# Optimization experiments

Hardware: AMD Instinct MI355X
Metric: run time of the kernel (lower is better)

Reference implementation:

```python
import jax, jax.numpy as jnp
import numpy as np


def _sin_rpe(Lq, d_model, dtype):
    # sinusoidal relative-position embeddings for positions -(Lq-1)..(Lq-1)
    inv_freq = 1.0 / (10000.0 ** (jnp.arange(0, d_model, 2, dtype=jnp.float32) / d_model))
    pos = jnp.arange(-(Lq - 1), Lq, dtype=jnp.float32)  # [2Lq-1]
    ang = pos[:, None] * inv_freq[None, :]               # [2Lq-1, d_model/2]
    emb = jnp.zeros((2 * Lq - 1, d_model), dtype=jnp.float32)
    emb = emb.at[:, 0::2].set(jnp.sin(ang)).at[:, 1::2].set(jnp.cos(ang))
    return emb.astype(dtype)


def _rel_shift(x):
    # Transformer-XL relative shift. x: [B,H,Lq,Lr] with Lr = 2Lq-1
    B, H, Lq, Lr = x.shape
    xp = jnp.concatenate([jnp.zeros((B, H, Lq, 1), x.dtype), x], axis=-1)
    xp = xp.reshape(B, H, Lr + 1, Lq)
    return xp[:, :, 1:].reshape(B, H, Lq, Lr)[..., Lr - Lq:]


def setup_inputs() -> dict:
    key = jax.random.key(0)
    ks = jax.random.split(key, 7)
    B, Lq, D, H = 1, 2048, 1024, 16
    d_head = D // H
    s = 0.02
    return {
        "w": jax.random.normal(ks[0], (B, Lq, D), jnp.float32),
        "Wq": jax.random.normal(ks[1], (D, D), jnp.float32) * s,
        "Wk": jax.random.normal(ks[2], (D, D), jnp.float32) * s,
        "Wv": jax.random.normal(ks[3], (D, D), jnp.float32) * s,
        "Wr": jax.random.normal(ks[4], (D, D), jnp.float32) * s,
        "u_bias": jax.random.normal(ks[5], (H, d_head), jnp.float32) * 0.02,
        "v_bias": jax.random.normal(ks[6], (H, d_head), jnp.float32) * 0.02,
    }


def reference(w, Wq, Wk, Wv, Wr, u_bias, v_bias):
    B, Lq, D = w.shape
    H, d_head = u_bias.shape
    scale = 1.0 / np.sqrt(d_head).astype(np.float32)
    r = _sin_rpe(Lq, D, w.dtype)                          # [2Lq-1, D]
    # torch Linear: y = x @ W.T
    q = (w @ Wq.T).reshape(B, Lq, H, d_head).transpose(0, 2, 1, 3)  # [B,H,Lq,d]
    k = (w @ Wk.T).reshape(B, Lq, H, d_head).transpose(0, 2, 1, 3)
    v = (w @ Wv.T).reshape(B, Lq, H, d_head).transpose(0, 2, 1, 3)
    rp = (r @ Wr.T).reshape(2 * Lq - 1, H, d_head).transpose(1, 0, 2)  # [H,2Lq-1,d]
    AC = jnp.einsum('bhid,bhjd->bhij', q + u_bias[None, :, None, :], k)   # [B,H,Lq,Lq]
    BD = jnp.einsum('bhid,hjd->bhij', q + v_bias[None, :, None, :], rp)   # [B,H,Lq,2Lq-1]
    BD = _rel_shift(BD)                                                   # [B,H,Lq,Lq]
    attn = jax.nn.softmax((AC + BD) * scale, axis=-1)
    out = jnp.einsum('bhij,bhjd->bhid', attn, v)          # [B,H,Lq,d]
    return out.transpose(0, 2, 1, 3).reshape(B, Lq, D)
```

## Files before the change

### kernel.cpp

```cpp
#include <hip/hip_runtime.h>
#include <math.h>
#include <stddef.h>

#define LQ 2048
#define DM 1024
#define NH 16
#define DH 64
#define LR 4095

typedef __attribute__((ext_vector_type(4))) float f4v;
typedef __attribute__((ext_vector_type(8))) short s8v;
typedef __attribute__((ext_vector_type(2))) unsigned short us2;
typedef __attribute__((ext_vector_type(8))) unsigned short us8;
typedef __attribute__((ext_vector_type(2))) unsigned int u32x2;
typedef __attribute__((ext_vector_type(4))) unsigned int u32x4;

__device__ __forceinline__ unsigned short f2bf(float x) {
    unsigned int u = __float_as_uint(x);
    return (unsigned short)((u + 0x7FFFu + ((u >> 16) & 1u)) >> 16);
}
__device__ __forceinline__ float bf2f(unsigned short s) {
    return __uint_as_float(((unsigned int)s) << 16);
}
__device__ __forceinline__ unsigned cvtpk(float lo, float hi) {
    unsigned r;
    asm("v_cvt_pk_bf16_f32 %0, %1, %2" : "=v"(r) : "v"(lo), "v"(hi));
    return r;
}
template<int CTRL>
__device__ __forceinline__ float rot16(float x) {
    return __uint_as_float((unsigned)__builtin_amdgcn_update_dpp(
        0, (int)__float_as_uint(x), CTRL, 0xF, 0xF, false));
}
#define GLOAD16(g, l) __builtin_amdgcn_global_load_lds((g), (l), 16, 0, 0)
#define WAVE_LDS_FENCE() do { \
    asm volatile("s_waitcnt lgkmcnt(0)" ::: "memory"); \
    __builtin_amdgcn_sched_barrier(0); } while (0)

#define MFMA16(a, b, c) __builtin_amdgcn_mfma_f32_16x16x32_bf16((a), (b), (c), 0, 0, 0)

__device__ __forceinline__ s8v sw_read8(const unsigned short* base, int row, int colshort) {
    int byte = (row * 128 + colshort * 2) ^ ((row & 7) << 4);
    return *(const s8v*)((const char*)base + byte);
}

__global__ __launch_bounds__(256)
void prep(const float* __restrict__ w, const float* __restrict__ Wq,
          const float* __restrict__ Wk, const float* __restrict__ Wv,
          const float* __restrict__ Wr, unsigned short* __restrict__ dst,
          unsigned short* __restrict__ r, unsigned short* __restrict__ rpg) {
    int b = blockIdx.x;
    if (b < 3072) {
        size_t e0 = ((size_t)b * 256 + threadIdx.x) * 8;
        const float* src;
        if (e0 < (size_t)LQ * DM) src = w + e0;
        else {
            size_t ro = e0 - (size_t)LQ * DM;
            int wi = (int)(ro >> 20);
            size_t off = ro & 1048575;
            src = (wi == 0 ? Wq : wi == 1 ? Wk : wi == 2 ? Wv : Wr) + off;
        }
        f4v a = *(const f4v*)src;
        f4v c = *(const f4v*)(src + 4);
        us8 o;
        o[0]=f2bf(a[0]); o[1]=f2bf(a[1]); o[2]=f2bf(a[2]); o[3]=f2bf(a[3]);
        o[4]=f2bf(c[0]); o[5]=f2bf(c[1]); o[6]=f2bf(c[2]); o[7]=f2bf(c[3]);
        *(us8*)(dst + e0) = o;
    } else if (b < 11262) {
        int tg = (b - 3072) * 256 + threadIdx.x;
        int gm = tg >> 9, c2 = tg & 511;
        float invf = expf(-(float)c2 * (9.210340371976184f / 512.0f));
        float ang = (float)(gm - (LQ - 1)) * invf;
        us2 o; o[0] = f2bf(sinf(ang)); o[1] = f2bf(cosf(ang));
        *(us2*)&r[(size_t)gm * DM + c2 * 2] = o;
    } else {
        int idx = (b - 11262) * 2048 + threadIdx.x * 8;
        unsigned short* p = (idx < 131072)
            ? (rpg - 131072 + idx)
            : (rpg + (size_t)LR * DM + (idx - 131072));
        *(us8*)p = (us8){0,0,0,0,0,0,0,0};
    }
}

__global__ __launch_bounds__(256)
void proj_all(const unsigned short* __restrict__ wbf, const unsigned short* __restrict__ rr,
              const unsigned short* __restrict__ Wqb, const unsigned short* __restrict__ Wkb,
              const unsigned short* __restrict__ Wvb, const unsigned short* __restrict__ Wrb,
              unsigned short* __restrict__ qb, unsigned short* __restrict__ kkb,
              unsigned short* __restrict__ vtg, unsigned short* __restrict__ rpg) {
    __shared__ unsigned short ldsbuf[2 * 128 * 64];
    unsigned short* As = ldsbuf;
    unsigned short* Bs = ldsbuf + 128 * 64;
    int bid = blockIdx.x;
    int mat, mblk, nblk;
    if (bid < 384) { mat = bid >> 7; int rm = bid & 127; mblk = rm >> 3; nblk = rm & 7; }
    else           { mat = 3; int rm = bid - 384; mblk = rm >> 3; nblk = rm & 7; }
    const int M = (mat < 3) ? LQ : LR;
    const unsigned short* A = (mat < 3) ? wbf : rr;
    const unsigned short* B = mat == 0 ? Wqb : mat == 1 ? Wkb : mat == 2 ? Wvb : Wrb;
    unsigned short* C = mat == 0 ? qb : mat == 1 ? kkb : mat == 2 ? vtg : rpg;
    const int m0 = mblk * 128, n0 = nblk * 128;
    const int t = threadIdx.x;
    const int w = t >> 6, lan16 = t & 15, lgrp = (t & 63) >> 4;
    const int wm = (w >> 1) * 64, wn = (w & 1) * 64;
    f4v acc[4][4] = {};

    for (int k0 = 0; k0 < DM; k0 += 64) {
        #pragma unroll
        for (int it = 0; it < 4; ++it) {
            int slot = it * 256 + t;
            int row = slot >> 3, c8 = slot & 7;
            int gm = m0 + row; if (gm > M - 1) gm = M - 1;
            GLOAD16(A + (size_t)gm * DM + k0 + c8 * 8,
                    (char*)As + (size_t)(it * 256 + (t & ~63)) * 16);
            GLOAD16(B + (size_t)(n0 + row) * DM + k0 + c8 * 8,
                    (char*)Bs + (size_t)(it * 256 + (t & ~63)) * 16);
        }
        __syncthreads();
        #pragma unroll
        for (int kk = 0; kk < 2; ++kk) {
            s8v aF[4], bF[4];
            #pragma unroll
            for (int i = 0; i < 4; ++i) {
                aF[i] = *(const s8v*)&As[(wm + i * 16 + lan16) * 64 + kk * 32 + lgrp * 8];
                bF[i] = *(const s8v*)&Bs[(wn + i * 16 + lan16) * 64 + kk * 32 + lgrp * 8];
            }
            #pragma unroll
            for (int i = 0; i < 4; ++i)
                #pragma unroll
                for (int j = 0; j < 4; ++j)
                    acc[i][j] = MFMA16(aF[i], bF[j], acc[i][j]);
        }
        __syncthreads();
    }
    if (mat != 2) {
        #pragma unroll
        for (int i = 0; i < 4; ++i)
            #pragma unroll
            for (int j = 0; j < 4; ++j)
                #pragma unroll
                for (int rg = 0; rg < 4; ++rg) {
                    int row = m0 + wm + i * 16 + lgrp * 4 + rg;
                    if (row < M)
                        C[(size_t)row * DM + n0 + wn + j * 16 + lan16] = f2bf(acc[i][j][rg]);
                }
    } else {
        unsigned short* Ct = ldsbuf;
        #pragma unroll
        for (int i = 0; i < 4; ++i)
            #pragma unroll
            for (int j = 0; j < 4; ++j) {
                int n = wn + j * 16 + lan16;
                int mb = wm + i * 16 + lgrp * 4;
                int byte = (n * 256 + mb * 2) ^ ((n & 7) << 4);
                u32x2 pp;
                pp[0] = cvtpk(acc[i][j][0], acc[i][j][1]);
                pp[1] = cvtpk(acc[i][j][2], acc[i][j][3]);
                *(u32x2*)((char*)Ct + byte) = pp;
            }
        __syncthreads();
        #pragma unroll
        for (int it = 0; it < 8; ++it) {
            int slot = it * 256 + t;
            int n = slot >> 4, c8 = slot & 15;
            int byte = (n * 256 + c8 * 16) ^ ((n & 7) << 4);
            us8 v = *(const us8*)((const char*)Ct + byte);
            *(us8*)&C[(size_t)(n0 + n) * LQ + m0 + c8 * 8] = v;
        }
    }
}

__global__ __launch_bounds__(256, 2)
void attn_mfma(const unsigned short* __restrict__ q, const unsigned short* __restrict__ kkg,
               const unsigned short* __restrict__ vtg, const unsigned short* __restrict__ rpg,
               const float* __restrict__ ub, const float* __restrict__ vb,
               float* __restrict__ out) {
    __shared__ unsigned short Kb[2][64 * 64];
    __shared__ unsigned short Bb[2][128 * 64];
    __shared__ unsigned short Vb[64 * 64];
    __shared__ unsigned short Gtw[4][80 * 20];
    __shared__ unsigned short Pt[4][64 * 18];

    const int dd = blockIdx.x;
    const int f = (dd & 7) * 64 + (dd >> 3);
    const int h = f >> 5;
    const int i0 = (f & 31) * 64;
    const int col0 = h * DH;

    const int t = threadIdx.x;
    const int w = t >> 6, lan16 = t & 15, lgrp = (t & 63) >> 4;
    const int W = w * 16;
    const int cbase = 48 - W;
    const float C1 = 0.125f * 1.4426950408889634f;
    const float C0 = -4.0f * 1.4426950408889634f;

    unsigned short* gw = Gtw[w];
    unsigned short* pw = Pt[w];

    union uv { u32x4 u; s8v s; };
    auto mkfrag = [&](int gi, const float* bias, s8v* dstf) {
        #pragma unroll
        for (int kk = 0; kk < 2; ++kk) {
            int cb = kk * 32 + lgrp * 8;
            us8 qv = (us8){0,0,0,0,0,0,0,0};
            if (gi < LQ) qv = *(const us8*)(q + (size_t)gi * DM + col0 + cb);
            f4v b0 = *(const f4v*)(bias + col0 + cb);
            f4v b1 = *(const f4v*)(bias + col0 + cb + 4);
            uv o;
            o.u[0] = cvtpk(bf2f(qv[0]) + b0[0], bf2f(qv[1]) + b0[1]);
            o.u[1] = cvtpk(bf2f(qv[2]) + b0[2], bf2f(qv[3]) + b0[3]);
            o.u[2] = cvtpk(bf2f(qv[4]) + b1[0], bf2f(qv[5]) + b1[1]);
            o.u[3] = cvtpk(bf2f(qv[6]) + b1[2], bf2f(qv[7]) + b1[3]);
            dstf[kk] = o.s;
        }
    };
    s8v quF[2], qvlF[2], qvsF[2];
    mkfrag(i0 + W + lan16, ub, quF);
    mkfrag(i0 + W + lan16, vb, qvlF);
    mkfrag(i0 + W + 1 + lan16, vb, qvsF);

    auto stageK = [&](int j0, int buf) {
        #pragma unroll
        for (int it = 0; it < 2; ++it) {
            int slot = it * 256 + t;
            int row = slot >> 3, c8 = (t & 7) ^ (row & 7);
            GLOAD16(kkg + (size_t)(j0 + row) * DM + col0 + c8 * 8,
                    (char*)&Kb[buf][0] + (size_t)(it * 256 + (t & ~63)) * 16);
        }
    };
    auto stageB = [&](int rel, int buf) {
        int base = (rel <= 0) ? rel + 4031 : rel - 65;
        #pragma unroll
        for (int it = 0; it < 4; ++it) {
            int slot = it * 256 + t;
            int row = slot >> 3, c8 = (t & 7) ^ (row & 7);
            GLOAD16(rpg + (ptrdiff_t)(base + row) * DM + col0 + c8 * 8,
                    (char*)&Bb[buf][0] + (size_t)(it * 256 + (t & ~63)) * 16);
        }
    };
    auto stageV = [&](int j0) {
        #pragma unroll
        for (int it = 0; it < 2; ++it) {
            int slot = it * 256 + t;
            int row = slot >> 3, c8 = (t & 7) ^ (row & 7);
            GLOAD16(vtg + (size_t)(col0 + row) * LQ + j0 + c8 * 8,
                    (char*)&Vb[0] + (size_t)(it * 256 + (t & ~63)) * 16);
        }
    };

    f4v accO[4] = {};
    float lsum[4] = {0.f, 0.f, 0.f, 0.f};

    stageK(0, 0);
    stageB(0 - i0, 0);

    auto tile_body = [&](int tt, int cur) {
        const int j0 = tt * 64;
        const int rel = j0 - i0;
        stageV(j0);
        const int tn = (tt < 31) ? tt + 1 : 31;
        stageK(tn * 64, cur ^ 1);
        stageB(tn * 64 - i0, cur ^ 1);
        __builtin_amdgcn_sched_barrier(0);
        asm volatile("s_waitcnt vmcnt(8)" ::: "memory");
        __builtin_amdgcn_s_barrier();
        __builtin_amdgcn_sched_barrier(0);

        __builtin_amdgcn_s_setprio(1);
        f4v acF[4] = {};
        #pragma unroll
        for (int nf = 0; nf < 4; ++nf)
            #pragma unroll
            for (int kk = 0; kk < 2; ++kk) {
                s8v bF = sw_read8(&Kb[cur][0], nf * 16 + lan16, kk * 32 + lgrp * 8);
                acF[nf] = MFMA16(quF[kk], bF, acF[nf]);
            }
        f4v g[5] = {};
        {
            const s8v* qf = (rel <= 0) ? qvlF : qvsF;
            #pragma unroll
            for (int c = 0; c < 5; ++c)
                #pragma unroll
                for (int kk = 0; kk < 2; ++kk) {
                    s8v bF = sw_read8(&Bb[cur][0], cbase + c * 16 + lan16, kk * 32 + lgrp * 8);
                    g[c] = MFMA16(qf[kk], bF, g[c]);
                }
        }
        __builtin_amdgcn_s_setprio(0);
        if (rel == 0) {
            #pragma unroll
            for (int c = 0; c < 5; ++c) {
                int trow = -65 + cbase + c * 16 + lan16;
                const unsigned short* bp = rpg + (ptrdiff_t)trow * DM + col0;
                #pragma unroll
                for (int kk = 0; kk < 2; ++kk) {
                    us8 bv = *(const us8*)(bp + kk * 32 + lgrp * 8);
                    g[c] = MFMA16(qvsF[kk], (s8v)bv, g[c]);
                }
            }
        }
        #pragma unroll
        for (int c = 0; c < 5; ++c) {
            int cl = c * 16 + lan16;
            u32x2 pp;
            pp[0] = cvtpk(g[c][0], g[c][1]);
            pp[1] = cvtpk(g[c][2], g[c][3]);
            *(u32x2*)&gw[cl * 20 + lgrp * 4] = pp;
        }
        WAVE_LDS_FENCE();

        #pragma unroll
        for (int nf = 0; nf < 4; ++nf) {
            int jl = nf * 16 + lan16;
            float pp[4];
            #pragma unroll
            for (int rg = 0; rg < 4; ++rg) {
                const int rhat = lgrp * 4 + rg;
                float bd = bf2f(gw[(jl - rhat + 15) * 20 + rhat]);
                pp[rg] = exp2f(fmaf(acF[nf][rg] + bd, C1, C0));
                lsum[rg] += pp[rg];
            }
            *(unsigned*)&pw[jl * 18 + lgrp * 4]     = cvtpk(pp[0], pp[1]);
            *(unsigned*)&pw[jl * 18 + lgrp * 4 + 2] = cvtpk(pp[2], pp[3]);
        }
        WAVE_LDS_FENCE();

        s8v pF[2];
        #pragma unroll
        for (int kk = 0; kk < 2; ++kk) {
            us8 tmp;
            #pragma unroll
            for (int e = 0; e < 8; ++e)
                tmp[e] = pw[(kk * 32 + lgrp * 8 + e) * 18 + lan16];
            pF[kk] = (s8v)tmp;
        }
        __builtin_amdgcn_sched_barrier(0);
        asm volatile("s_waitcnt vmcnt(6)" ::: "memory");
        __builtin_amdgcn_s_barrier();
        __builtin_amdgcn_sched_barrier(0);

        __builtin_amdgcn_s_setprio(1);
        #pragma unroll
        for (int nf = 0; nf < 4; ++nf)
            #pragma unroll
            for (int kk = 0; kk < 2; ++kk) {
                s8v vF = sw_read8(&Vb[0], nf * 16 + lan16, kk * 32 + lgrp * 8);
                accO[nf] = MFMA16(pF[kk], vF, accO[nf]);
            }
        __builtin_amdgcn_s_setprio(0);
        __builtin_amdgcn_sched_barrier(0);
        __builtin_amdgcn_s_barrier();
        __builtin_amdgcn_sched_barrier(0);
    };

    #pragma unroll 1
    for (int tp = 0; tp < 16; ++tp) {
        tile_body(tp * 2, 0);
        tile_body(tp * 2 + 1, 1);
    }

    #pragma unroll
    for (int rg = 0; rg < 4; ++rg) {
        float s = lsum[rg];
        s += rot16<0x121>(s);
        s += rot16<0x122>(s);
        s += rot16<0x124>(s);
        s += rot16<0x128>(s);
        float inv = 1.f / s;
        const int row = i0 + W + lgrp * 4 + rg;
        #pragma unroll
        for (int nf = 0; nf < 4; ++nf)
            out[(size_t)row * DM + col0 + nf * 16 + lan16] = accO[nf][rg] * inv;
    }
}

extern "C" void kernel_launch(void* const* d_in, const int* in_sizes, int n_in,
                              void* d_out, int out_size, void* d_ws, size_t ws_size,
                              hipStream_t stream) {
    const float* w  = (const float*)d_in[0];
    const float* Wq = (const float*)d_in[1];
    const float* Wk = (const float*)d_in[2];
    const float* Wv = (const float*)d_in[3];
    const float* Wr = (const float*)d_in[4];
    const float* ub = (const float*)d_in[5];
    const float* vb = (const float*)d_in[6];
    float* out = (float*)d_out;

    const size_t U = 1048576;
    unsigned short* ws = (unsigned short*)d_ws;
    unsigned short* wbf = ws;
    unsigned short* Wqb = ws + 2 * U;
    unsigned short* Wkb = ws + 3 * U;
    unsigned short* Wvb = ws + 4 * U;
    unsigned short* Wrb = ws + 5 * U;
    unsigned short* qb  = ws + 6 * U;
    unsigned short* kkb = ws + 8 * U;
    unsigned short* vtg = ws + 10 * U;
    unsigned short* rpg = ws + 12 * U + 131072;
    unsigned short* r   = rpg + (size_t)LR * DM + 131072;

    dim3 blk(256);
    hipLaunchKernelGGL(prep, dim3(11390), blk, 0, stream, w, Wq, Wk, Wv, Wr, wbf, r, rpg);
    hipLaunchKernelGGL(proj_all, dim3(640), blk, 0, stream,
                       wbf, r, Wqb, Wkb, Wvb, Wrb, qb, kkb, vtg, rpg);
    hipLaunchKernelGGL(attn_mfma, dim3(512), blk, 0, stream,
                       qb, kkb, vtg, rpg, ub, vb, out);
}
```

Measured before the change: 130.9 us.

## Transpose MFMA operand order so scores land row-per-lane, simplifying P and BD LDS paths

Swaps the A/B operands of every MFMA in the attention kernel so each lane holds a query row's scores across columns, instead of a column across rows. The BD shift buffer and probability buffer are relaid out to match. P fragments now come from a single 16-byte LDS read rather than eight scalar gathers, the row sum becomes one scalar per lane, and the final reduction uses two shuffles. It also uses sincosf in the prep kernel. The aim is to cut LDS instructions and scalar traffic in the softmax section, at the cost of a changed LDS layout whose strides may now cause bank conflicts.

```diff
diff --git a/kernel.cpp b/kernel.cpp
--- a/kernel.cpp
+++ b/kernel.cpp
@@ -26,11 +26,6 @@
     unsigned r;
     asm("v_cvt_pk_bf16_f32 %0, %1, %2" : "=v"(r) : "v"(lo), "v"(hi));
     return r;
-}
-template<int CTRL>
-__device__ __forceinline__ float rot16(float x) {
-    return __uint_as_float((unsigned)__builtin_amdgcn_update_dpp(
-        0, (int)__float_as_uint(x), CTRL, 0xF, 0xF, false));
 }
 #define GLOAD16(g, l) __builtin_amdgcn_global_load_lds((g), (l), 16, 0, 0)
 #define WAVE_LDS_FENCE() do { \
@@ -71,7 +66,9 @@
         int gm = tg >> 9, c2 = tg & 511;
         float invf = expf(-(float)c2 * (9.210340371976184f / 512.0f));
         float ang = (float)(gm - (LQ - 1)) * invf;
-        us2 o; o[0] = f2bf(sinf(ang)); o[1] = f2bf(cosf(ang));
+        float sv, cv;
+        sincosf(ang, &sv, &cv);
+        us2 o; o[0] = f2bf(sv); o[1] = f2bf(cv);
         *(us2*)&r[(size_t)gm * DM + c2 * 2] = o;
     } else {
         int idx = (b - 11262) * 2048 + threadIdx.x * 8;
@@ -178,8 +175,8 @@
     __shared__ unsigned short Kb[2][64 * 64];
     __shared__ unsigned short Bb[2][128 * 64];
     __shared__ unsigned short Vb[64 * 64];
-    __shared__ unsigned short Gtw[4][80 * 20];
-    __shared__ unsigned short Pt[4][64 * 18];
+    __shared__ unsigned short Gtw[4][16 * 84];
+    __shared__ unsigned short Ptw[4][16 * 72];
 
     const int dd = blockIdx.x;
     const int f = (dd & 7) * 64 + (dd >> 3);
@@ -195,7 +192,7 @@
     const float C0 = -4.0f * 1.4426950408889634f;
 
     unsigned short* gw = Gtw[w];
-    unsigned short* pw = Pt[w];
+    unsigned short* pw = Ptw[w];
 
     union uv { u32x4 u; s8v s; };
     auto mkfrag = [&](int gi, const float* bias, s8v* dstf) {
@@ -249,7 +246,7 @@
     };
 
     f4v accO[4] = {};
-    float lsum[4] = {0.f, 0.f, 0.f, 0.f};
+    float lsum = 0.f;
 
     stageK(0, 0);
     stageB(0 - i0, 0);
@@ -273,7 +270,7 @@
             #pragma unroll
             for (int kk = 0; kk < 2; ++kk) {
                 s8v bF = sw_read8(&Kb[cur][0], nf * 16 + lan16, kk * 32 + lgrp * 8);
-                acF[nf] = MFMA16(quF[kk], bF, acF[nf]);
+                acF[nf] = MFMA16(bF, quF[kk], acF[nf]);
             }
         f4v g[5] = {};
         {
@@ -283,7 +280,7 @@
                 #pragma unroll
                 for (int kk = 0; kk < 2; ++kk) {
                     s8v bF = sw_read8(&Bb[cur][0], cbase + c * 16 + lan16, kk * 32 + lgrp * 8);
-                    g[c] = MFMA16(qf[kk], bF, g[c]);
+                    g[c] = MFMA16(bF, qf[kk], g[c]);
                 }
         }
         __builtin_amdgcn_s_setprio(0);
@@ -295,45 +292,40 @@
                 #pragma unroll
                 for (int kk = 0; kk < 2; ++kk) {
                     us8 bv = *(const us8*)(bp + kk * 32 + lgrp * 8);
-                    g[c] = MFMA16(qvsF[kk], (s8v)bv, g[c]);
+                    g[c] = MFMA16((s8v)bv, qvsF[kk], g[c]);
                 }
             }
         }
         #pragma unroll
         for (int c = 0; c < 5; ++c) {
-            int cl = c * 16 + lan16;
             u32x2 pp;
             pp[0] = cvtpk(g[c][0], g[c][1]);
             pp[1] = cvtpk(g[c][2], g[c][3]);
-            *(u32x2*)&gw[cl * 20 + lgrp * 4] = pp;
+            *(u32x2*)&gw[lan16 * 84 + c * 16 + lgrp * 4] = pp;
         }
         WAVE_LDS_FENCE();
 
         #pragma unroll
         for (int nf = 0; nf < 4; ++nf) {
-            int jl = nf * 16 + lan16;
-            float pp[4];
+            float pr[4];
             #pragma unroll
             for (int rg = 0; rg < 4; ++rg) {
-                const int rhat = lgrp * 4 + rg;
-                float bd = bf2f(gw[(jl - rhat + 15) * 20 + rhat]);
-                pp[rg] = exp2f(fmaf(acF[nf][rg] + bd, C1, C0));
-                lsum[rg] += pp[rg];
-            }
-            *(unsigned*)&pw[jl * 18 + lgrp * 4]     = cvtpk(pp[0], pp[1]);
-            *(unsigned*)&pw[jl * 18 + lgrp * 4 + 2] = cvtpk(pp[2], pp[3]);
+                int j = nf * 16 + lgrp * 4 + rg;
+                float bd = bf2f(gw[lan16 * 83 + j + 15]);
+                pr[rg] = exp2f(fmaf(acF[nf][rg] + bd, C1, C0));
+                lsum += pr[rg];
+            }
+            u32x2 pp;
+            pp[0] = cvtpk(pr[0], pr[1]);
+            pp[1] = cvtpk(pr[2], pr[3]);
+            *(u32x2*)&pw[lan16 * 72 + nf * 16 + lgrp * 4] = pp;
         }
         WAVE_LDS_FENCE();
 
         s8v pF[2];
         #pragma unroll
-        for (int kk = 0; kk < 2; ++kk) {
-            us8 tmp;
-            #pragma unroll
-            for (int e = 0; e < 8; ++e)
-                tmp[e] = pw[(kk * 32 + lgrp * 8 + e) * 18 + lan16];
-            pF[kk] = (s8v)tmp;
-        }
+        for (int kk = 0; kk < 2; ++kk)
+            pF[kk] = *(const s8v*)&pw[lan16 * 72 + kk * 32 + lgrp * 8];
         __builtin_amdgcn_sched_barrier(0);
         asm volatile("s_waitcnt vmcnt(6)" ::: "memory");
         __builtin_amdgcn_s_barrier();
@@ -345,7 +337,7 @@
             #pragma unroll
             for (int kk = 0; kk < 2; ++kk) {
                 s8v vF = sw_read8(&Vb[0], nf * 16 + lan16, kk * 32 + lgrp * 8);
-                accO[nf] = MFMA16(pF[kk], vF, accO[nf]);
+                accO[nf] = MFMA16(vF, pF[kk], accO[nf]);
             }
         __builtin_amdgcn_s_setprio(0);
         __builtin_amdgcn_sched_barrier(0);
@@ -359,19 +351,16 @@
         tile_body(tp * 2 + 1, 1);
     }
 
+    float s = lsum;
+    s += __shfl_xor(s, 16, 64);
+    s += __shfl_xor(s, 32, 64);
+    float inv = 1.f / s;
+    const int row = i0 + W + lan16;
     #pragma unroll
-    for (int rg = 0; rg < 4; ++rg) {
-        float s = lsum[rg];
-        s += rot16<0x121>(s);
-        s += rot16<0x122>(s);
-        s += rot16<0x124>(s);
-        s += rot16<0x128>(s);
-        float inv = 1.f / s;
-        const int row = i0 + W + lgrp * 4 + rg;
-        #pragma unroll
-        for (int nf = 0; nf < 4; ++nf)
-            out[(size_t)row * DM + col0 + nf * 16 + lan16] = accO[nf][rg] * inv;
-    }
+    for (int nf = 0; nf < 4; ++nf)
+        #pragma unroll
+        for (int rg = 0; rg < 4; ++rg)
+            out[(size_t)row * DM + col0 + nf * 16 + lgrp * 4 + rg] = accO[nf][rg] * inv;
 }
 
 extern "C" void kernel_launch(void* const* d_in, const int* in_sizes, int n_in,
```

Measured after the change: 137.4 us. +5.0%, slower.
